# Performance work log

Hardware: AMD Instinct MI355X
Metric: run time of the kernel (lower is better)

The kernel has to match this reference:

```python
import jax, jax.numpy as jnp
import numpy as np

N, E, K = 50000, 800000, 16
D, H = 128, 8
DH = D // H
SCALE = D ** (-0.5)
EPS = 1e-5


def _ln(x, g, b):
    m = jnp.mean(x, axis=-1, keepdims=True)
    v = jnp.mean((x - m) ** 2, axis=-1, keepdims=True)
    return (x - m) * jax.lax.rsqrt(v + EPS) * g + b


def setup_inputs() -> dict:
    key = jax.random.key(0)
    ks = jax.random.split(key, 20)
    s = 0.02
    inp = {
        "triplet_h": jax.random.normal(ks[0], (N, D), jnp.float32),
        "mask_nodes": jnp.ones((N,), jnp.bool_),
        "src": jax.random.randint(ks[1], (E,), 0, N),
        "dst": jax.random.randint(ks[2], (E,), 0, N),
        "edge_bias": jax.random.normal(ks[3], (E, H), jnp.float32),
        "mask_edges": jnp.ones((E,), jnp.bool_),
        "inc_idx": jax.random.randint(ks[4], (N, K), 0, E),
        "inc_mask": jnp.ones((N, K), jnp.bool_),
        # params
        "ln1_g": jnp.ones((D,), jnp.float32),
        "ln1_b": jnp.zeros((D,), jnp.float32),
        "qkv_w": jax.random.normal(ks[5], (D, 3 * D), jnp.float32) * s,
        "qkv_b": jnp.zeros((3 * D,), jnp.float32),
        "res_in_w": jax.random.normal(ks[6], (D, D), jnp.float32) * s,
        "res_in_b": jnp.zeros((D,), jnp.float32),
        "res_ln_g": jnp.ones((D,), jnp.float32),
        "res_ln_b": jnp.zeros((D,), jnp.float32),
        "ffn_in_w": jax.random.normal(ks[7], (D, 4 * D), jnp.float32) * s,
        "ffn_in_b": jnp.zeros((4 * D,), jnp.float32),
        "ffn_out_w": jax.random.normal(ks[8], (4 * D, D), jnp.float32) * s,
        "ffn_out_b": jnp.zeros((D,), jnp.float32),
    }
    return inp


def reference(triplet_h, mask_nodes, src, dst, edge_bias, mask_edges, inc_idx,
              inc_mask, ln1_g, ln1_b, qkv_w, qkv_b, res_in_w, res_in_b,
              res_ln_g, res_ln_b, ffn_in_w, ffn_in_b, ffn_out_w, ffn_out_b):
    x = _ln(triplet_h, ln1_g, ln1_b)
    qkv = (x @ qkv_w + qkv_b).reshape(-1, 3, H, DH)
    q = qkv[:, 0] * SCALE  # [N,H,dh]
    k = qkv[:, 1]
    v = qkv[:, 2]

    zero_i = jnp.zeros_like(src)
    se = jnp.where(mask_edges, src, zero_i)
    de = jnp.where(mask_edges, dst, zero_i)

    dot_all = jnp.sum(q[se] * k[de], axis=-1)  # [E,H]
    me = mask_edges[:, None]
    dot_all = jnp.where(me, dot_all, 0.0)
    eb = jnp.where(me, edge_bias, 0.0)
    scores_all = dot_all + eb  # [E,H]

    v_src = jnp.where(me[:, :, None], v[se], 0.0)  # [E,H,dh]

    idx = jnp.clip(inc_idx, 0)  # [N,K]
    s_in = scores_all[idx]  # [N,K,H]
    v_in = v_src[idx]       # [N,K,H,dh]
    m_in = inc_mask & mask_nodes[:, None]
    s_in = jnp.where(m_in[:, :, None], s_in, -1e9)
    a_in = jax.nn.softmax(s_in, axis=1)  # [N,K,H]
    out = jnp.sum(v_in * a_in[..., None], axis=1).reshape(-1, H * DH)  # [N,D]

    # Residual block (dropout p=0)
    x2 = triplet_h + (out @ res_in_w + res_in_b)
    y = _ln(x2, res_ln_g, res_ln_b)
    y = jax.nn.gelu(y @ ffn_in_w + ffn_in_b) @ ffn_out_w + ffn_out_b
    return x2 + y
```

## Files before the change

kernel.cpp:

```cpp
#include <hip/hip_runtime.h>
#include <math.h>

#define N_NODES 50000
#define N_EDGES 800000
#define QSCALE 0.08838834764831845f
#define LEPS 1e-5f

typedef unsigned short ushort_t;
typedef unsigned char uchar_t;
typedef short bf16x8 __attribute__((ext_vector_type(8)));
typedef float f32x4 __attribute__((ext_vector_type(4)));
typedef float f32x2 __attribute__((ext_vector_type(2)));

__device__ __forceinline__ ushort_t f2b(float f) {
    unsigned int u = __float_as_uint(f);
    u += 0x7FFF + ((u >> 16) & 1);
    return (ushort_t)(u >> 16);
}
__device__ __forceinline__ uchar_t f2fp8(float f) {
    unsigned int pk = __builtin_amdgcn_cvt_pk_fp8_f32(f, f, 0, false);
    return (uchar_t)(pk & 0xff);
}
__device__ __forceinline__ float gelu_f(float x) {
    const float c = 0.7978845608028654f;
    float x3 = x * x * x;
    return 0.5f * x * (1.f + tanhf(c * (x + 0.044715f * x3)));
}
__device__ __forceinline__ void gload16(const ushort_t* g, ushort_t* l) {
    __builtin_amdgcn_global_load_lds(
        (const __attribute__((address_space(1))) unsigned int*)g,
        (__attribute__((address_space(3))) unsigned int*)l, 16, 0, 0);
}
__device__ __forceinline__ int frag_idx(int n7, int k7) {
    return ((n7 >> 4) * 4 + (k7 >> 5)) * 512 + ((k7 >> 3) & 3) * 128 + (n7 & 15) * 8 + (k7 & 7);
}

__global__ __launch_bounds__(256) void k_prep(
    const float* __restrict__ qkvw, const float* __restrict__ riw,
    const float* __restrict__ fiw,  const float* __restrict__ fow,
    ushort_t* __restrict__ qkvwT, ushort_t* __restrict__ riwT,
    ushort_t* __restrict__ fiwT,  ushort_t* __restrict__ fowT)
{
    int i = blockIdx.x * 256 + threadIdx.x;
    if (i < 384 * 128) {
        int n = i >> 7, k = i & 127;
        qkvwT[(size_t)(n >> 7) * 16384 + frag_idx(n & 127, k)] = f2b(qkvw[k * 384 + n]);
        return;
    }
    i -= 384 * 128;
    if (i < 128 * 128) {
        int n = i >> 7, k = i & 127;
        riwT[frag_idx(n, k)] = f2b(riw[k * 128 + n]);
        return;
    }
    i -= 128 * 128;
    if (i < 512 * 128) {
        int n = i >> 7, k = i & 127;
        fiwT[(size_t)(n >> 7) * 16384 + frag_idx(n & 127, k)] = f2b(fiw[k * 512 + n]);
        return;
    }
    i -= 512 * 128;
    if (i < 128 * 512) {
        int n = i >> 9, k = i & 511;
        fowT[(size_t)(k >> 7) * 16384 + frag_idx(n, k & 127)] = f2b(fow[k * 128 + n]);
    }
}

__global__ __launch_bounds__(256) void k1_ln_qkv(
    const float* __restrict__ th, const float* __restrict__ g1, const float* __restrict__ b1,
    const ushort_t* __restrict__ wT, const float* __restrict__ bias,
    uchar_t* __restrict__ q8, uchar_t* __restrict__ k8, uchar_t* __restrict__ v8)
{
    __shared__ __align__(16) ushort_t xs[64][136];
    __shared__ __align__(16) ushort_t wbuf[16384];
    const int tid = threadIdx.x, lane = tid & 63, w = tid >> 6;
    const int g0 = blockIdx.x * 64;
    const bf16x8* wb8 = (const bf16x8*)wbuf;

    #pragma unroll
    for (int t = 0; t < 8; ++t)
        gload16(wT + (size_t)(t * 256 + tid) * 8, wbuf + (t * 256 + tid) * 8);

    float ga = g1[lane], gb = g1[lane + 64];
    float ba = b1[lane], bb = b1[lane + 64];
    for (int rr = 0; rr < 16; ++rr) {
        int r = w * 16 + rr, grow = g0 + r;
        float x0 = 0.f, x1 = 0.f;
        if (grow < N_NODES) {
            x0 = th[(size_t)grow * 128 + lane];
            x1 = th[(size_t)grow * 128 + 64 + lane];
        }
        float s1 = x0 + x1, s2 = x0 * x0 + x1 * x1;
        #pragma unroll
        for (int off = 32; off; off >>= 1) { s1 += __shfl_xor(s1, off); s2 += __shfl_xor(s2, off); }
        float m = s1 * (1.f / 128.f);
        float v = s2 * (1.f / 128.f) - m * m;
        float rs = rsqrtf(v + LEPS);
        xs[r][lane]      = f2b((x0 - m) * rs * ga + ba);
        xs[r][lane + 64] = f2b((x1 - m) * rs * gb + bb);
    }
    __syncthreads();

    const int q = lane >> 4, ml = lane & 15;
    bf16x8 a[4];
    #pragma unroll
    for (int kc = 0; kc < 4; ++kc)
        a[kc] = *(const bf16x8*)&xs[w * 16 + ml][kc * 32 + q * 8];
    const int rbase = g0 + w * 16 + q * 4;

    for (int ch = 0; ch < 3; ++ch) {
        if (ch) {
            __syncthreads();
            #pragma unroll
            for (int t = 0; t < 8; ++t)
                gload16(wT + (size_t)ch * 16384 + (t * 256 + tid) * 8, wbuf + (t * 256 + tid) * 8);
            __syncthreads();
        } else {
            __syncthreads();
        }
        uchar_t* outp = (ch == 0) ? q8 : (ch == 1) ? k8 : v8;
        #pragma unroll
        for (int t2 = 0; t2 < 8; ++t2) {
            int n = t2 * 16 + ml;
            f32x4 acc = {0.f, 0.f, 0.f, 0.f};
            #pragma unroll
            for (int kc = 0; kc < 4; ++kc)
                acc = __builtin_amdgcn_mfma_f32_16x16x32_bf16(
                    a[kc], wb8[(t2 * 4 + kc) * 64 + lane], acc, 0, 0, 0);
            float bs = bias[ch * 128 + n];
            #pragma unroll
            for (int r = 0; r < 4; ++r) {
                int grow = rbase + r;
                if (grow < N_NODES)
                    outp[(size_t)grow * 128 + n] = f2fp8(acc[r] + bs);
            }
        }
    }
}

__global__ __launch_bounds__(256) void k23_agg(
    const uchar_t* __restrict__ q8, const uchar_t* __restrict__ k8,
    const uchar_t* __restrict__ v8,
    const int* __restrict__ src, const int* __restrict__ dst,
    const int* __restrict__ inc_idx, const float* __restrict__ eb,
    ushort_t* __restrict__ outw)
{
    __shared__ int es[32];
    __shared__ int ss[32];
    __shared__ int ds[32];
    __shared__ float sc[2][16][8];
    const int tid = threadIdx.x;
    const int nb = blockIdx.x * 2;

    if (tid < 32) {
        int n = nb + (tid >> 4);
        int e = inc_idx[(size_t)n * 16 + (tid & 15)];
        if (e < 0) e = 0;
        es[tid] = e;
        ss[tid] = src[e];
        ds[tid] = dst[e];
    }
    __syncthreads();
    {
        int pair = tid >> 3, h = tid & 7;
        int e = es[pair], s = ss[pair], d = ds[pair];
        uint4 qa = *(const uint4*)(q8 + (size_t)s * 128 + h * 16);
        uint4 ka = *(const uint4*)(k8 + (size_t)d * 128 + h * 16);
        const unsigned int* qu = (const unsigned int*)&qa;
        const unsigned int* ku = (const unsigned int*)&ka;
        float acc = 0.f;
        #pragma unroll
        for (int j = 0; j < 4; ++j) {
            f32x2 q0 = __builtin_amdgcn_cvt_pk_f32_fp8(qu[j], false);
            f32x2 q1 = __builtin_amdgcn_cvt_pk_f32_fp8(qu[j], true);
            f32x2 k0 = __builtin_amdgcn_cvt_pk_f32_fp8(ku[j], false);
            f32x2 k1 = __builtin_amdgcn_cvt_pk_f32_fp8(ku[j], true);
            acc = fmaf(q0.x, k0.x, acc); acc = fmaf(q0.y, k0.y, acc);
            acc = fmaf(q1.x, k1.x, acc); acc = fmaf(q1.y, k1.y, acc);
        }
        sc[pair >> 4][pair & 15][h] = acc * QSCALE + eb[(size_t)e * 8 + h];
    }
    __syncthreads();

    const int loc = tid >> 7;
    const int j = tid & 127;
    const int h = j >> 4;
    float m = -1e30f;
    #pragma unroll
    for (int k = 0; k < 16; k++) m = fmaxf(m, sc[loc][k][h]);
    float p[16];
    float sum = 0.f;
    #pragma unroll
    for (int k = 0; k < 16; k++) { p[k] = __expf(sc[loc][k][h] - m); sum += p[k]; }
    float inv = 1.f / sum;
    float acc = 0.f;
    #pragma unroll
    for (int k = 0; k < 16; k++)
        acc += p[k] * __builtin_amdgcn_cvt_f32_fp8((int)v8[(size_t)ss[loc * 16 + k] * 128 + j], 0);
    outw[(size_t)(nb + loc) * 128 + j] = f2b(acc * inv);
}

__global__ __launch_bounds__(256) void k4_ffn(
    const float* __restrict__ th, const ushort_t* __restrict__ outw,
    const ushort_t* __restrict__ riwT, const float* __restrict__ rib,
    const float* __restrict__ rlg, const float* __restrict__ rlb,
    const ushort_t* __restrict__ fiwT, const float* __restrict__ fib,
    const ushort_t* __restrict__ fowT, const float* __restrict__ fob,
    float* __restrict__ dout)
{
    __shared__ __align__(16) ushort_t ys[64][136];
    __shared__ __align__(16) ushort_t hs[64][136];
    __shared__ __align__(16) ushort_t wbuf[16384];
    const int tid = threadIdx.x, lane = tid & 63, w = tid >> 6;
    const int g0 = blockIdx.x * 64;
    const int q = lane >> 4, ml = lane & 15;
    const int rloc = w * 16 + q * 4;
    const int aswz = (ml >> 2) & 3;
    const bf16x8* wb8 = (const bf16x8*)wbuf;

    #pragma unroll
    for (int t = 0; t < 8; ++t)
        gload16(riwT + (size_t)(t * 256 + tid) * 8, wbuf + (t * 256 + tid) * 8);

    int arow = g0 + w * 16 + ml; if (arow > N_NODES - 1) arow = N_NODES - 1;
    bf16x8 a[4];
    #pragma unroll
    for (int kc = 0; kc < 4; ++kc)
        a[kc] = *(const bf16x8*)(outw + (size_t)arow * 128 + kc * 32 + q * 8);
    __syncthreads();

    f32x4 x2[8];
    #pragma unroll
    for (int t = 0; t < 8; ++t) {
        f32x4 acc = {0.f, 0.f, 0.f, 0.f};
        #pragma unroll
        for (int kc = 0; kc < 4; ++kc)
            acc = __builtin_amdgcn_mfma_f32_16x16x32_bf16(
                a[kc], wb8[(t * 4 + kc) * 64 + lane], acc, 0, 0, 0);
        x2[t] = acc;
    }
    #pragma unroll
    for (int t = 0; t < 8; ++t) {
        float bb = rib[t * 16 + ml];
        #pragma unroll
        for (int r = 0; r < 4; ++r) {
            int grow = g0 + rloc + r;
            float tv = (grow < N_NODES) ? th[(size_t)grow * 128 + t * 16 + ml] : 0.f;
            x2[t][r] += bb + tv;
        }
    }

    {
        float rg[8], rbv[8];
        #pragma unroll
        for (int t = 0; t < 8; ++t) { rg[t] = rlg[t * 16 + ml]; rbv[t] = rlb[t * 16 + ml]; }
        #pragma unroll
        for (int r = 0; r < 4; ++r) {
            float s1 = 0.f, s2 = 0.f;
            #pragma unroll
            for (int t = 0; t < 8; ++t) { float v = x2[t][r]; s1 += v; s2 += v * v; }
            #pragma unroll
            for (int off = 1; off < 16; off <<= 1) { s1 += __shfl_xor(s1, off); s2 += __shfl_xor(s2, off); }
            float m = s1 * (1.f / 128.f);
            float v = s2 * (1.f / 128.f) - m * m;
            float rs = rsqrtf(v + LEPS);
            #pragma unroll
            for (int t = 0; t < 8; ++t) {
                int G = (2 * t + (ml >> 3)) ^ q;
                ys[rloc + r][G * 8 + (ml & 7)] = f2b((x2[t][r] - m) * rs * rg[t] + rbv[t]);
            }
        }
    }
    __syncthreads();

    bf16x8 a2[4];
    #pragma unroll
    for (int kc = 0; kc < 4; ++kc)
        a2[kc] = *(const bf16x8*)&ys[w * 16 + ml][(((kc * 4 + q) ^ aswz) << 3)];

    f32x4 y2[8];
    #pragma unroll
    for (int t = 0; t < 8; ++t) y2[t] = (f32x4){0.f, 0.f, 0.f, 0.f};

    for (int c4 = 0; c4 < 4; ++c4) {
        #pragma unroll
        for (int t = 0; t < 8; ++t)
            gload16(fiwT + (size_t)c4 * 16384 + (t * 256 + tid) * 8, wbuf + (t * 256 + tid) * 8);
        __syncthreads();
        #pragma unroll
        for (int t2 = 0; t2 < 8; ++t2) {
            f32x4 hacc = {0.f, 0.f, 0.f, 0.f};
            #pragma unroll
            for (int kc = 0; kc < 4; ++kc)
                hacc = __builtin_amdgcn_mfma_f32_16x16x32_bf16(
                    a2[kc], wb8[(t2 * 4 + kc) * 64 + lane], hacc, 0, 0, 0);
            float fb = fib[c4 * 128 + t2 * 16 + ml];
            int G = (2 * t2 + (ml >> 3)) ^ q;
            #pragma unroll
            for (int r = 0; r < 4; ++r)
                hs[rloc + r][G * 8 + (ml & 7)] = f2b(gelu_f(hacc[r] + fb));
        }
        __syncthreads();
        #pragma unroll
        for (int t = 0; t < 8; ++t)
            gload16(fowT + (size_t)c4 * 16384 + (t * 256 + tid) * 8, wbuf + (t * 256 + tid) * 8);
        __syncthreads();
        bf16x8 a3[4];
        #pragma unroll
        for (int kc = 0; kc < 4; ++kc)
            a3[kc] = *(const bf16x8*)&hs[w * 16 + ml][(((kc * 4 + q) ^ aswz) << 3)];
        #pragma unroll
        for (int t = 0; t < 8; ++t) {
            #pragma unroll
            for (int kc = 0; kc < 4; ++kc)
                y2[t] = __builtin_amdgcn_mfma_f32_16x16x32_bf16(
                    a3[kc], wb8[(t * 4 + kc) * 64 + lane], y2[t], 0, 0, 0);
        }
        __syncthreads();
    }

    #pragma unroll
    for (int t = 0; t < 8; ++t) {
        float ob = fob[t * 16 + ml];
        #pragma unroll
        for (int r = 0; r < 4; ++r) {
            int grow = g0 + rloc + r;
            if (grow < N_NODES)
                dout[(size_t)grow * 128 + t * 16 + ml] = x2[t][r] + y2[t][r] + ob;
        }
    }
}

extern "C" void kernel_launch(void* const* d_in, const int* in_sizes, int n_in,
                              void* d_out, int out_size, void* d_ws, size_t ws_size,
                              hipStream_t stream)
{
    const float* th    = (const float*)d_in[0];
    const int*   src   = (const int*)d_in[2];
    const int*   dst   = (const int*)d_in[3];
    const float* ebias = (const float*)d_in[4];
    const int*   inc   = (const int*)d_in[6];
    const float* ln1g  = (const float*)d_in[8];
    const float* ln1b  = (const float*)d_in[9];
    const float* qkvw  = (const float*)d_in[10];
    const float* qkvb  = (const float*)d_in[11];
    const float* riw   = (const float*)d_in[12];
    const float* rib   = (const float*)d_in[13];
    const float* rlg   = (const float*)d_in[14];
    const float* rlb   = (const float*)d_in[15];
    const float* fiw   = (const float*)d_in[16];
    const float* fib   = (const float*)d_in[17];
    const float* fow   = (const float*)d_in[18];
    const float* fob   = (const float*)d_in[19];

    char* ws = (char*)d_ws;
    uchar_t* q8      = (uchar_t*)ws;                               ws += (size_t)N_NODES * 128;
    uchar_t* k8      = (uchar_t*)ws;                               ws += (size_t)N_NODES * 128;
    uchar_t* v8      = (uchar_t*)ws;                               ws += (size_t)N_NODES * 128;
    ushort_t* outw   = (ushort_t*)ws;                              ws += (size_t)N_NODES * 128 * 2;
    ushort_t* qkvwT  = (ushort_t*)ws;                              ws += (size_t)384 * 128 * 2;
    ushort_t* riwT   = (ushort_t*)ws;                              ws += (size_t)128 * 128 * 2;
    ushort_t* fiwT   = (ushort_t*)ws;                              ws += (size_t)512 * 128 * 2;
    ushort_t* fowT   = (ushort_t*)ws;                              ws += (size_t)128 * 512 * 2;
    float* dout = (float*)d_out;

    k_prep<<<768, 256, 0, stream>>>(qkvw, riw, fiw, fow, qkvwT, riwT, fiwT, fowT);
    k1_ln_qkv<<<(N_NODES + 63) / 64, 256, 0, stream>>>(th, ln1g, ln1b, qkvwT, qkvb, q8, k8, v8);
    k23_agg<<<N_NODES / 2, 256, 0, stream>>>(q8, k8, v8, src, dst, inc, ebias, outw);
    k4_ffn<<<(N_NODES + 63) / 64, 256, 0, stream>>>(th, outw, riwT, rib, rlg, rlb,
                                                    fiwT, fib, fowT, fob, dout);
}
```

Measured before the change: 315.1 us.

## Halve LDS in QKV and FFN kernels, stage fp8 outputs for coalesced stores

The QKV kernel now loads each 128-column weight chunk in two 64-wide K halves, which halves its weight LDS buffer. It writes fp8 results into the freed xs buffer and then stores whole rows with 16-byte writes instead of scattered byte stores. The FFN kernel shares one activation buffer for the LN output and the GELU hidden tile, and moves a barrier to the top of the loop. GELU replaces tanhf with an __expf-based form. Together these aim to cut LDS use for higher occupancy, improve store coalescing and cheapen GELU, at the cost of extra barriers in the QKV kernel.

```diff
diff --git a/kernel.cpp b/kernel.cpp
--- a/kernel.cpp
+++ b/kernel.cpp
@@ -22,9 +22,10 @@
     return (uchar_t)(pk & 0xff);
 }
 __device__ __forceinline__ float gelu_f(float x) {
-    const float c = 0.7978845608028654f;
-    float x3 = x * x * x;
-    return 0.5f * x * (1.f + tanhf(c * (x + 0.044715f * x3)));
+    float u = 1.5957691216057308f * (x + 0.044715f * x * x * x);
+    float e = __expf(u);
+    float t = 1.f - 2.f / (e + 1.f);
+    return 0.5f * x * (1.f + t);
 }
 __device__ __forceinline__ void gload16(const ushort_t* g, ushort_t* l) {
     __builtin_amdgcn_global_load_lds(
@@ -33,6 +34,9 @@
 }
 __device__ __forceinline__ int frag_idx(int n7, int k7) {
     return ((n7 >> 4) * 4 + (k7 >> 5)) * 512 + ((k7 >> 3) & 3) * 128 + (n7 & 15) * 8 + (k7 & 7);
+}
+__device__ __forceinline__ int fidx64(int n7, int k6) {
+    return ((n7 >> 4) * 2 + (k6 >> 5)) * 512 + ((k6 >> 3) & 3) * 128 + (n7 & 15) * 8 + (k6 & 7);
 }
 
 __global__ __launch_bounds__(256) void k_prep(
@@ -44,7 +48,8 @@
     int i = blockIdx.x * 256 + threadIdx.x;
     if (i < 384 * 128) {
         int n = i >> 7, k = i & 127;
-        qkvwT[(size_t)(n >> 7) * 16384 + frag_idx(n & 127, k)] = f2b(qkvw[k * 384 + n]);
+        int ch = n >> 7, n7 = n & 127, half = k >> 6, k6 = k & 63;
+        qkvwT[(size_t)(ch * 2 + half) * 8192 + fidx64(n7, k6)] = f2b(qkvw[k * 384 + n]);
         return;
     }
     i -= 384 * 128;
@@ -72,14 +77,11 @@
     uchar_t* __restrict__ q8, uchar_t* __restrict__ k8, uchar_t* __restrict__ v8)
 {
     __shared__ __align__(16) ushort_t xs[64][136];
-    __shared__ __align__(16) ushort_t wbuf[16384];
+    __shared__ __align__(16) ushort_t wbuf[8192];
     const int tid = threadIdx.x, lane = tid & 63, w = tid >> 6;
     const int g0 = blockIdx.x * 64;
     const bf16x8* wb8 = (const bf16x8*)wbuf;
-
-    #pragma unroll
-    for (int t = 0; t < 8; ++t)
-        gload16(wT + (size_t)(t * 256 + tid) * 8, wbuf + (t * 256 + tid) * 8);
+    uchar_t* sbuf8 = (uchar_t*)xs;
 
     float ga = g1[lane], gb = g1[lane + 64];
     float ba = b1[lane], bb = b1[lane + 64];
@@ -102,38 +104,47 @@
     __syncthreads();
 
     const int q = lane >> 4, ml = lane & 15;
+    const int rloc = w * 16 + q * 4;
     bf16x8 a[4];
     #pragma unroll
     for (int kc = 0; kc < 4; ++kc)
         a[kc] = *(const bf16x8*)&xs[w * 16 + ml][kc * 32 + q * 8];
-    const int rbase = g0 + w * 16 + q * 4;
 
     for (int ch = 0; ch < 3; ++ch) {
-        if (ch) {
+        f32x4 acc[8];
+        #pragma unroll
+        for (int t2 = 0; t2 < 8; ++t2) acc[t2] = (f32x4){0.f, 0.f, 0.f, 0.f};
+        #pragma unroll
+        for (int half = 0; half < 2; ++half) {
             __syncthreads();
             #pragma unroll
-            for (int t = 0; t < 8; ++t)
-                gload16(wT + (size_t)ch * 16384 + (t * 256 + tid) * 8, wbuf + (t * 256 + tid) * 8);
+            for (int t = 0; t < 4; ++t)
+                gload16(wT + (size_t)(ch * 2 + half) * 8192 + (t * 256 + tid) * 8,
+                        wbuf + (t * 256 + tid) * 8);
             __syncthreads();
-        } else {
-            __syncthreads();
-        }
-        uchar_t* outp = (ch == 0) ? q8 : (ch == 1) ? k8 : v8;
+            #pragma unroll
+            for (int t2 = 0; t2 < 8; ++t2)
+                #pragma unroll
+                for (int kc2 = 0; kc2 < 2; ++kc2)
+                    acc[t2] = __builtin_amdgcn_mfma_f32_16x16x32_bf16(
+                        a[half * 2 + kc2], wb8[(t2 * 2 + kc2) * 64 + lane], acc[t2], 0, 0, 0);
+        }
         #pragma unroll
         for (int t2 = 0; t2 < 8; ++t2) {
             int n = t2 * 16 + ml;
-            f32x4 acc = {0.f, 0.f, 0.f, 0.f};
-            #pragma unroll
-            for (int kc = 0; kc < 4; ++kc)
-                acc = __builtin_amdgcn_mfma_f32_16x16x32_bf16(
-                    a[kc], wb8[(t2 * 4 + kc) * 64 + lane], acc, 0, 0, 0);
             float bs = bias[ch * 128 + n];
             #pragma unroll
-            for (int r = 0; r < 4; ++r) {
-                int grow = rbase + r;
-                if (grow < N_NODES)
-                    outp[(size_t)grow * 128 + n] = f2fp8(acc[r] + bs);
-            }
+            for (int r = 0; r < 4; ++r)
+                sbuf8[(rloc + r) * 128 + n] = f2fp8(acc[t2][r] + bs);
+        }
+        __syncthreads();
+        uchar_t* outp = (ch == 0) ? q8 : (ch == 1) ? k8 : v8;
+        int grow = g0 + (tid >> 2);
+        if (grow < N_NODES) {
+            uint4 v0 = *(const uint4*)(sbuf8 + tid * 32);
+            uint4 v1 = *(const uint4*)(sbuf8 + tid * 32 + 16);
+            *(uint4*)(outp + (size_t)grow * 128 + (tid & 3) * 32) = v0;
+            *(uint4*)(outp + (size_t)grow * 128 + (tid & 3) * 32 + 16) = v1;
         }
     }
 }
@@ -208,8 +219,7 @@
     const ushort_t* __restrict__ fowT, const float* __restrict__ fob,
     float* __restrict__ dout)
 {
-    __shared__ __align__(16) ushort_t ys[64][136];
-    __shared__ __align__(16) ushort_t hs[64][136];
+    __shared__ __align__(16) ushort_t sbuf[64][136];
     __shared__ __align__(16) ushort_t wbuf[16384];
     const int tid = threadIdx.x, lane = tid & 63, w = tid >> 6;
     const int g0 = blockIdx.x * 64;
@@ -267,7 +277,7 @@
             #pragma unroll
             for (int t = 0; t < 8; ++t) {
                 int G = (2 * t + (ml >> 3)) ^ q;
-                ys[rloc + r][G * 8 + (ml & 7)] = f2b((x2[t][r] - m) * rs * rg[t] + rbv[t]);
+                sbuf[rloc + r][G * 8 + (ml & 7)] = f2b((x2[t][r] - m) * rs * rg[t] + rbv[t]);
             }
         }
     }
@@ -276,13 +286,14 @@
     bf16x8 a2[4];
     #pragma unroll
     for (int kc = 0; kc < 4; ++kc)
-        a2[kc] = *(const bf16x8*)&ys[w * 16 + ml][(((kc * 4 + q) ^ aswz) << 3)];
+        a2[kc] = *(const bf16x8*)&sbuf[w * 16 + ml][(((kc * 4 + q) ^ aswz) << 3)];
 
     f32x4 y2[8];
     #pragma unroll
     for (int t = 0; t < 8; ++t) y2[t] = (f32x4){0.f, 0.f, 0.f, 0.f};
 
     for (int c4 = 0; c4 < 4; ++c4) {
+        __syncthreads();
         #pragma unroll
         for (int t = 0; t < 8; ++t)
             gload16(fiwT + (size_t)c4 * 16384 + (t * 256 + tid) * 8, wbuf + (t * 256 + tid) * 8);
@@ -298,7 +309,7 @@
             int G = (2 * t2 + (ml >> 3)) ^ q;
             #pragma unroll
             for (int r = 0; r < 4; ++r)
-                hs[rloc + r][G * 8 + (ml & 7)] = f2b(gelu_f(hacc[r] + fb));
+                sbuf[rloc + r][G * 8 + (ml & 7)] = f2b(gelu_f(hacc[r] + fb));
         }
         __syncthreads();
         #pragma unroll
@@ -308,7 +319,7 @@
         bf16x8 a3[4];
         #pragma unroll
         for (int kc = 0; kc < 4; ++kc)
-            a3[kc] = *(const bf16x8*)&hs[w * 16 + ml][(((kc * 4 + q) ^ aswz) << 3)];
+            a3[kc] = *(const bf16x8*)&sbuf[w * 16 + ml][(((kc * 4 + q) ^ aswz) << 3)];
         #pragma unroll
         for (int t = 0; t < 8; ++t) {
             #pragma unroll
@@ -316,7 +327,6 @@
                 y2[t] = __builtin_amdgcn_mfma_f32_16x16x32_bf16(
                     a3[kc], wb8[(t * 4 + kc) * 64 + lane], y2[t], 0, 0, 0);
         }
-        __syncthreads();
     }
 
     #pragma unroll
```

Measured after the change: 289.5 us. 8.1% less time.
